# Kernel tuning notes

Hardware: AMD Instinct MI355X
Metric: run time of the kernel (lower is better)

## Reference

```python
import jax, jax.numpy as jnp
import numpy as np

W = 4096          # n_wavelengths
S = 4096          # n_spatial_modes
N_KEYS = 1024     # number of stored memories
SHARPNESS = 10.0  # config.retrieval_sharpness


def setup_inputs() -> dict:
    key = jax.random.key(0)
    k = jax.random.split(key, 6)
    return {
        "holo_re": jax.random.normal(k[0], (W, S), dtype=jnp.float32),
        "holo_im": jax.random.normal(k[1], (W, S), dtype=jnp.float32),
        "cue_re": jax.random.normal(k[2], (W, S), dtype=jnp.float32),
        "cue_im": jax.random.normal(k[3], (W, S), dtype=jnp.float32),
        "keys_re": jax.random.normal(k[4], (N_KEYS, W), dtype=jnp.float32),
        "keys_im": jax.random.normal(k[5], (N_KEYS, W), dtype=jnp.float32),
    }


def reference(holo_re, holo_im, cue_re, cue_im, keys_re, keys_im):
    hologram = holo_re + 1j * holo_im      # [W, S] complex64
    cue = cue_re + 1j * cue_im             # [W, S]
    keys = keys_re + 1j * keys_im          # [N, W]
    # noisy_mix = (hologram * cue.conj()).sum(dim=1)
    noisy_mix = jnp.sum(hologram * jnp.conj(cue), axis=1)  # [W]
    # torch.dot does NOT conjugate: plain complex dot per key -> batched matvec
    correlations = jnp.abs(keys @ noisy_mix)               # [N]
    attention = jax.nn.softmax(correlations * SHARPNESS)   # [N] real
    clean_key = attention.astype(keys.dtype) @ keys        # [W] complex
    out = hologram * clean_key[:, None]                    # [W, S] complex
    # return real/imag stacked so the harness compares real arrays
    return jnp.stack([out.real, out.imag])                 # [2, W, S] float32
```

## Files before the change

kernel.cpp:

```cpp
#include <hip/hip_runtime.h>
#include <math.h>

#define WDIM 4096
#define SDIM 4096
#define NKEYS 1024
#define SHARP 10.0f

typedef float v4 __attribute__((ext_vector_type(4)));

__device__ __forceinline__ float wave_reduce_sum(float v) {
#pragma unroll
    for (int off = 32; off > 0; off >>= 1) v += __shfl_down(v, off, 64);
    return v;
}

__global__ __launch_bounds__(256) void k_mix(
    const float* __restrict__ hr, const float* __restrict__ hi,
    const float* __restrict__ cr, const float* __restrict__ ci,
    float* __restrict__ mix_re, float* __restrict__ mix_im) {
    const int wave = threadIdx.x >> 6, lane = threadIdx.x & 63;
    const int w = blockIdx.x * 4 + wave;
    const size_t base = (size_t)w * SDIM;
    const v4* hr4 = (const v4*)(hr + base);
    const v4* hi4 = (const v4*)(hi + base);
    const v4* cr4 = (const v4*)(cr + base);
    const v4* ci4 = (const v4*)(ci + base);
    float sr = 0.f, si = 0.f;
#pragma unroll 1
    for (int it = 0; it < 4; ++it) {
        v4 a[4], b[4], c[4], d[4];
#pragma unroll
        for (int j = 0; j < 4; ++j) {
            const int idx = it * 256 + j * 64 + lane;
            a[j] = hr4[idx];
            b[j] = hi4[idx];
            c[j] = __builtin_nontemporal_load(cr4 + idx);
            d[j] = __builtin_nontemporal_load(ci4 + idx);
        }
#pragma unroll
        for (int j = 0; j < 4; ++j) {
            sr += a[j].x * c[j].x + b[j].x * d[j].x;  si += b[j].x * c[j].x - a[j].x * d[j].x;
            sr += a[j].y * c[j].y + b[j].y * d[j].y;  si += b[j].y * c[j].y - a[j].y * d[j].y;
            sr += a[j].z * c[j].z + b[j].z * d[j].z;  si += b[j].z * c[j].z - a[j].z * d[j].z;
            sr += a[j].w * c[j].w + b[j].w * d[j].w;  si += b[j].w * c[j].w - a[j].w * d[j].w;
        }
    }
    sr = wave_reduce_sum(sr);
    si = wave_reduce_sum(si);
    if (lane == 0) { mix_re[w] = sr; mix_im[w] = si; }
}

__global__ __launch_bounds__(256) void k_corr(
    const float* __restrict__ kr, const float* __restrict__ ki,
    const float* __restrict__ mr, const float* __restrict__ mi,
    float* __restrict__ corr) {
    const int wave = threadIdx.x >> 6, lane = threadIdx.x & 63;
    const int n = blockIdx.x * 4 + wave;
    const size_t base = (size_t)n * WDIM;
    const v4* kr4 = (const v4*)(kr + base);
    const v4* ki4 = (const v4*)(ki + base);
    const v4* mr4 = (const v4*)mr;
    const v4* mi4 = (const v4*)mi;
    float zr = 0.f, zi = 0.f;
#pragma unroll 1
    for (int it = 0; it < 4; ++it) {
        v4 a[4], b[4], m[4], q[4];
#pragma unroll
        for (int j = 0; j < 4; ++j) {
            const int idx = it * 256 + j * 64 + lane;
            a[j] = kr4[idx];
            b[j] = ki4[idx];
            m[j] = mr4[idx];
            q[j] = mi4[idx];
        }
#pragma unroll
        for (int j = 0; j < 4; ++j) {
            zr += a[j].x * m[j].x - b[j].x * q[j].x;  zi += a[j].x * q[j].x + b[j].x * m[j].x;
            zr += a[j].y * m[j].y - b[j].y * q[j].y;  zi += a[j].y * q[j].y + b[j].y * m[j].y;
            zr += a[j].z * m[j].z - b[j].z * q[j].z;  zi += a[j].z * q[j].z + b[j].z * m[j].z;
            zr += a[j].w * m[j].w - b[j].w * q[j].w;  zi += a[j].w * q[j].w + b[j].w * m[j].w;
        }
    }
    zr = wave_reduce_sum(zr);
    zi = wave_reduce_sum(zi);
    if (lane == 0) corr[n] = sqrtf(zr * zr + zi * zi) * SHARP;
}

__global__ __launch_bounds__(256) void k_softmax(
    const float* __restrict__ corr, float* __restrict__ att) {
    const int t = threadIdx.x;
    __shared__ float red[256];
    float v[4];
    float m = -1e30f;
#pragma unroll
    for (int j = 0; j < 4; ++j) { v[j] = corr[t + j * 256]; m = fmaxf(m, v[j]); }
    red[t] = m; __syncthreads();
    for (int s = 128; s > 0; s >>= 1) {
        if (t < s) red[t] = fmaxf(red[t], red[t + s]);
        __syncthreads();
    }
    const float mx = red[0];
    __syncthreads();
    float e[4]; float sum = 0.f;
#pragma unroll
    for (int j = 0; j < 4; ++j) { e[j] = expf(v[j] - mx); sum += e[j]; }
    red[t] = sum; __syncthreads();
    for (int s = 128; s > 0; s >>= 1) {
        if (t < s) red[t] += red[t + s];
        __syncthreads();
    }
    const float inv = 1.0f / red[0];
#pragma unroll
    for (int j = 0; j < 4; ++j) att[t + j * 256] = e[j] * inv;
}

__global__ __launch_bounds__(256) void k_clean(
    const float* __restrict__ kr, const float* __restrict__ ki,
    const float* __restrict__ att,
    float* __restrict__ clean_re, float* __restrict__ clean_im) {
    const int wt = blockIdx.x;
    const int nc = blockIdx.y;
    const int f4 = wt * 256 + threadIdx.x;
    const int n0 = nc * 16;
    float arx = 0.f, ary = 0.f, arz = 0.f, arw = 0.f;
    float aix = 0.f, aiy = 0.f, aiz = 0.f, aiw = 0.f;
#pragma unroll 1
    for (int jt = 0; jt < 4; ++jt) {
        v4 x[4], y[4]; float a[4];
#pragma unroll
        for (int j = 0; j < 4; ++j) {
            const int n = n0 + jt * 4 + j;
            a[j] = att[n];
            x[j] = ((const v4*)(kr + (size_t)n * WDIM))[f4];
            y[j] = ((const v4*)(ki + (size_t)n * WDIM))[f4];
        }
#pragma unroll
        for (int j = 0; j < 4; ++j) {
            arx += a[j] * x[j].x; ary += a[j] * x[j].y; arz += a[j] * x[j].z; arw += a[j] * x[j].w;
            aix += a[j] * y[j].x; aiy += a[j] * y[j].y; aiz += a[j] * y[j].z; aiw += a[j] * y[j].w;
        }
    }
    const int w = f4 * 4;
    atomicAdd(&clean_re[w + 0], arx); atomicAdd(&clean_re[w + 1], ary);
    atomicAdd(&clean_re[w + 2], arz); atomicAdd(&clean_re[w + 3], arw);
    atomicAdd(&clean_im[w + 0], aix); atomicAdd(&clean_im[w + 1], aiy);
    atomicAdd(&clean_im[w + 2], aiz); atomicAdd(&clean_im[w + 3], aiw);
}

__global__ __launch_bounds__(256) void k_out(
    const float* __restrict__ hr, const float* __restrict__ hi,
    const float* __restrict__ cre, const float* __restrict__ cim,
    float* __restrict__ out_re, float* __restrict__ out_im) {
    const int w = blockIdx.x;
    const size_t base = (size_t)w * SDIM;
    const float a = cre[w], b = cim[w];
    const v4* hr4 = (const v4*)(hr + base);
    const v4* hi4 = (const v4*)(hi + base);
    v4* or4 = (v4*)(out_re + base);
    v4* oi4 = (v4*)(out_im + base);
    v4 h[4], g[4];
#pragma unroll
    for (int j = 0; j < 4; ++j) {
        const int i = threadIdx.x + j * 256;
        h[j] = hr4[i];
        g[j] = hi4[i];
    }
#pragma unroll
    for (int j = 0; j < 4; ++j) {
        const int i = threadIdx.x + j * 256;
        v4 orr, oii;
        orr.x = h[j].x * a - g[j].x * b;  oii.x = h[j].x * b + g[j].x * a;
        orr.y = h[j].y * a - g[j].y * b;  oii.y = h[j].y * b + g[j].y * a;
        orr.z = h[j].z * a - g[j].z * b;  oii.z = h[j].z * b + g[j].z * a;
        orr.w = h[j].w * a - g[j].w * b;  oii.w = h[j].w * b + g[j].w * a;
        __builtin_nontemporal_store(orr, or4 + i);
        __builtin_nontemporal_store(oii, oi4 + i);
    }
}

extern "C" void kernel_launch(void* const* d_in, const int* in_sizes, int n_in,
                              void* d_out, int out_size, void* d_ws, size_t ws_size,
                              hipStream_t stream) {
    const float* hr = (const float*)d_in[0];
    const float* hi = (const float*)d_in[1];
    const float* cr = (const float*)d_in[2];
    const float* ci = (const float*)d_in[3];
    const float* kr = (const float*)d_in[4];
    const float* ki = (const float*)d_in[5];

    float* ws = (float*)d_ws;
    float* mix_re = ws;
    float* mix_im = ws + 4096;
    float* corr   = ws + 8192;
    float* att    = ws + 9216;
    float* cre    = ws + 10240;
    float* cim    = ws + 14336;

    float* out_re = (float*)d_out;
    float* out_im = out_re + (size_t)WDIM * SDIM;

    k_mix<<<WDIM / 4, 256, 0, stream>>>(hr, hi, cr, ci, mix_re, mix_im);
    k_corr<<<NKEYS / 4, 256, 0, stream>>>(kr, ki, mix_re, mix_im, corr);
    k_softmax<<<1, 256, 0, stream>>>(corr, att);
    hipMemsetAsync(cre, 0, 2 * WDIM * sizeof(float), stream);
    k_clean<<<dim3(4, 64), 256, 0, stream>>>(kr, ki, att, cre, cim);
    k_out<<<WDIM, 256, 0, stream>>>(hr, hi, cre, cim, out_re, out_im);
}
```

Before: 379.1 us.

## Fuse softmax into clean-key kernel and use one block per row in reductions

The single-block softmax kernel is removed. Each k_clean block now recomputes the max and sum over all 1024 correlations itself and builds its 16 attention weights in shared memory, which saves one launch and the serial single-block step. k_mix and k_corr now assign one row per 256-thread block instead of one row per wave, with all loads issued up front and a shared-memory cross-wave reduction, giving more blocks and more memory requests in flight. The cost is redundant softmax work repeated in every k_clean block and an extra barrier in each reduction kernel.

```diff
diff --git a/kernel.cpp b/kernel.cpp
--- a/kernel.cpp
+++ b/kernel.cpp
@@ -18,82 +18,93 @@
     const float* __restrict__ hr, const float* __restrict__ hi,
     const float* __restrict__ cr, const float* __restrict__ ci,
     float* __restrict__ mix_re, float* __restrict__ mix_im) {
-    const int wave = threadIdx.x >> 6, lane = threadIdx.x & 63;
-    const int w = blockIdx.x * 4 + wave;
+    const int w = blockIdx.x;
+    const int t = threadIdx.x;
+    const int wave = t >> 6, lane = t & 63;
     const size_t base = (size_t)w * SDIM;
     const v4* hr4 = (const v4*)(hr + base);
     const v4* hi4 = (const v4*)(hi + base);
     const v4* cr4 = (const v4*)(cr + base);
     const v4* ci4 = (const v4*)(ci + base);
+    v4 a[4], b[4], c[4], d[4];
+#pragma unroll
+    for (int j = 0; j < 4; ++j) {
+        const int idx = t + j * 256;
+        a[j] = hr4[idx];
+        b[j] = hi4[idx];
+        c[j] = __builtin_nontemporal_load(cr4 + idx);
+        d[j] = __builtin_nontemporal_load(ci4 + idx);
+    }
     float sr = 0.f, si = 0.f;
-#pragma unroll 1
-    for (int it = 0; it < 4; ++it) {
-        v4 a[4], b[4], c[4], d[4];
-#pragma unroll
-        for (int j = 0; j < 4; ++j) {
-            const int idx = it * 256 + j * 64 + lane;
-            a[j] = hr4[idx];
-            b[j] = hi4[idx];
-            c[j] = __builtin_nontemporal_load(cr4 + idx);
-            d[j] = __builtin_nontemporal_load(ci4 + idx);
-        }
-#pragma unroll
-        for (int j = 0; j < 4; ++j) {
-            sr += a[j].x * c[j].x + b[j].x * d[j].x;  si += b[j].x * c[j].x - a[j].x * d[j].x;
-            sr += a[j].y * c[j].y + b[j].y * d[j].y;  si += b[j].y * c[j].y - a[j].y * d[j].y;
-            sr += a[j].z * c[j].z + b[j].z * d[j].z;  si += b[j].z * c[j].z - a[j].z * d[j].z;
-            sr += a[j].w * c[j].w + b[j].w * d[j].w;  si += b[j].w * c[j].w - a[j].w * d[j].w;
-        }
+#pragma unroll
+    for (int j = 0; j < 4; ++j) {
+        sr += a[j].x * c[j].x + b[j].x * d[j].x;  si += b[j].x * c[j].x - a[j].x * d[j].x;
+        sr += a[j].y * c[j].y + b[j].y * d[j].y;  si += b[j].y * c[j].y - a[j].y * d[j].y;
+        sr += a[j].z * c[j].z + b[j].z * d[j].z;  si += b[j].z * c[j].z - a[j].z * d[j].z;
+        sr += a[j].w * c[j].w + b[j].w * d[j].w;  si += b[j].w * c[j].w - a[j].w * d[j].w;
     }
     sr = wave_reduce_sum(sr);
     si = wave_reduce_sum(si);
-    if (lane == 0) { mix_re[w] = sr; mix_im[w] = si; }
+    __shared__ float rr[4], ri[4];
+    if (lane == 0) { rr[wave] = sr; ri[wave] = si; }
+    __syncthreads();
+    if (t == 0) {
+        mix_re[w] = rr[0] + rr[1] + rr[2] + rr[3];
+        mix_im[w] = ri[0] + ri[1] + ri[2] + ri[3];
+    }
 }
 
 __global__ __launch_bounds__(256) void k_corr(
     const float* __restrict__ kr, const float* __restrict__ ki,
     const float* __restrict__ mr, const float* __restrict__ mi,
     float* __restrict__ corr) {
-    const int wave = threadIdx.x >> 6, lane = threadIdx.x & 63;
-    const int n = blockIdx.x * 4 + wave;
+    const int n = blockIdx.x;
+    const int t = threadIdx.x;
+    const int wave = t >> 6, lane = t & 63;
     const size_t base = (size_t)n * WDIM;
     const v4* kr4 = (const v4*)(kr + base);
     const v4* ki4 = (const v4*)(ki + base);
     const v4* mr4 = (const v4*)mr;
     const v4* mi4 = (const v4*)mi;
+    v4 a[4], b[4], m[4], q[4];
+#pragma unroll
+    for (int j = 0; j < 4; ++j) {
+        const int idx = t + j * 256;
+        a[j] = kr4[idx];
+        b[j] = ki4[idx];
+        m[j] = mr4[idx];
+        q[j] = mi4[idx];
+    }
     float zr = 0.f, zi = 0.f;
-#pragma unroll 1
-    for (int it = 0; it < 4; ++it) {
-        v4 a[4], b[4], m[4], q[4];
-#pragma unroll
-        for (int j = 0; j < 4; ++j) {
-            const int idx = it * 256 + j * 64 + lane;
-            a[j] = kr4[idx];
-            b[j] = ki4[idx];
-            m[j] = mr4[idx];
-            q[j] = mi4[idx];
-        }
-#pragma unroll
-        for (int j = 0; j < 4; ++j) {
-            zr += a[j].x * m[j].x - b[j].x * q[j].x;  zi += a[j].x * q[j].x + b[j].x * m[j].x;
-            zr += a[j].y * m[j].y - b[j].y * q[j].y;  zi += a[j].y * q[j].y + b[j].y * m[j].y;
-            zr += a[j].z * m[j].z - b[j].z * q[j].z;  zi += a[j].z * q[j].z + b[j].z * m[j].z;
-            zr += a[j].w * m[j].w - b[j].w * q[j].w;  zi += a[j].w * q[j].w + b[j].w * m[j].w;
-        }
+#pragma unroll
+    for (int j = 0; j < 4; ++j) {
+        zr += a[j].x * m[j].x - b[j].x * q[j].x;  zi += a[j].x * q[j].x + b[j].x * m[j].x;
+        zr += a[j].y * m[j].y - b[j].y * q[j].y;  zi += a[j].y * q[j].y + b[j].y * m[j].y;
+        zr += a[j].z * m[j].z - b[j].z * q[j].z;  zi += a[j].z * q[j].z + b[j].z * m[j].z;
+        zr += a[j].w * m[j].w - b[j].w * q[j].w;  zi += a[j].w * q[j].w + b[j].w * m[j].w;
     }
     zr = wave_reduce_sum(zr);
     zi = wave_reduce_sum(zi);
-    if (lane == 0) corr[n] = sqrtf(zr * zr + zi * zi) * SHARP;
-}
-
-__global__ __launch_bounds__(256) void k_softmax(
-    const float* __restrict__ corr, float* __restrict__ att) {
+    __shared__ float rr[4], ri[4];
+    if (lane == 0) { rr[wave] = zr; ri[wave] = zi; }
+    __syncthreads();
+    if (t == 0) {
+        const float fr = rr[0] + rr[1] + rr[2] + rr[3];
+        const float fi = ri[0] + ri[1] + ri[2] + ri[3];
+        corr[n] = sqrtf(fr * fr + fi * fi) * SHARP;
+    }
+}
+
+__global__ __launch_bounds__(256) void k_clean(
+    const float* __restrict__ kr, const float* __restrict__ ki,
+    const float* __restrict__ corr,
+    float* __restrict__ clean_re, float* __restrict__ clean_im) {
     const int t = threadIdx.x;
     __shared__ float red[256];
-    float v[4];
-    float m = -1e30f;
-#pragma unroll
-    for (int j = 0; j < 4; ++j) { v[j] = corr[t + j * 256]; m = fmaxf(m, v[j]); }
+    __shared__ float satt[16];
+
+    float v0 = corr[t], v1 = corr[t + 256], v2 = corr[t + 512], v3 = corr[t + 768];
+    float m = fmaxf(fmaxf(v0, v1), fmaxf(v2, v3));
     red[t] = m; __syncthreads();
     for (int s = 128; s > 0; s >>= 1) {
         if (t < s) red[t] = fmaxf(red[t], red[t + s]);
@@ -101,27 +112,19 @@
     }
     const float mx = red[0];
     __syncthreads();
-    float e[4]; float sum = 0.f;
-#pragma unroll
-    for (int j = 0; j < 4; ++j) { e[j] = expf(v[j] - mx); sum += e[j]; }
+    float sum = expf(v0 - mx) + expf(v1 - mx) + expf(v2 - mx) + expf(v3 - mx);
     red[t] = sum; __syncthreads();
     for (int s = 128; s > 0; s >>= 1) {
         if (t < s) red[t] += red[t + s];
         __syncthreads();
     }
     const float inv = 1.0f / red[0];
-#pragma unroll
-    for (int j = 0; j < 4; ++j) att[t + j * 256] = e[j] * inv;
-}
-
-__global__ __launch_bounds__(256) void k_clean(
-    const float* __restrict__ kr, const float* __restrict__ ki,
-    const float* __restrict__ att,
-    float* __restrict__ clean_re, float* __restrict__ clean_im) {
+    const int n0 = blockIdx.y * 16;
+    if (t < 16) satt[t] = expf(corr[n0 + t] - mx) * inv;
+    __syncthreads();
+
     const int wt = blockIdx.x;
-    const int nc = blockIdx.y;
-    const int f4 = wt * 256 + threadIdx.x;
-    const int n0 = nc * 16;
+    const int f4 = wt * 256 + t;
     float arx = 0.f, ary = 0.f, arz = 0.f, arw = 0.f;
     float aix = 0.f, aiy = 0.f, aiz = 0.f, aiw = 0.f;
 #pragma unroll 1
@@ -130,7 +133,7 @@
 #pragma unroll
         for (int j = 0; j < 4; ++j) {
             const int n = n0 + jt * 4 + j;
-            a[j] = att[n];
+            a[j] = satt[jt * 4 + j];
             x[j] = ((const v4*)(kr + (size_t)n * WDIM))[f4];
             y[j] = ((const v4*)(ki + (size_t)n * WDIM))[f4];
         }
@@ -192,17 +195,15 @@
     float* mix_re = ws;
     float* mix_im = ws + 4096;
     float* corr   = ws + 8192;
-    float* att    = ws + 9216;
     float* cre    = ws + 10240;
     float* cim    = ws + 14336;
 
     float* out_re = (float*)d_out;
     float* out_im = out_re + (size_t)WDIM * SDIM;
 
-    k_mix<<<WDIM / 4, 256, 0, stream>>>(hr, hi, cr, ci, mix_re, mix_im);
-    k_corr<<<NKEYS / 4, 256, 0, stream>>>(kr, ki, mix_re, mix_im, corr);
-    k_softmax<<<1, 256, 0, stream>>>(corr, att);
     hipMemsetAsync(cre, 0, 2 * WDIM * sizeof(float), stream);
-    k_clean<<<dim3(4, 64), 256, 0, stream>>>(kr, ki, att, cre, cim);
+    k_mix<<<WDIM, 256, 0, stream>>>(hr, hi, cr, ci, mix_re, mix_im);
+    k_corr<<<NKEYS, 256, 0, stream>>>(kr, ki, mix_re, mix_im, corr);
+    k_clean<<<dim3(4, 64), 256, 0, stream>>>(kr, ki, corr, cre, cim);
     k_out<<<WDIM, 256, 0, stream>>>(hr, hi, cre, cim, out_re, out_im);
 }
```

New measurement: 364.9 us. 3.7% less time.
